# Performance work log

Measured on AMD Instinct MI355X. Metric: run time of the kernel, lower is better.

The kernel has to match this reference:

```python
import jax, jax.numpy as jnp
import numpy as np

N_NODES = 50000
N_EDGES = 800000
MUL = 32            # multiplicity of 0e and 1o feature irreps
N_SPECIES = 4       # node_attr = 4x0e one-hot
N_BASIS = 8         # radial basis scalars
N_HID = 8           # invariant_neurons
AVG_NEIGH = 16.0
INV_SQRT3 = 1.0 / np.sqrt(3.0).astype(np.float32)


def setup_inputs() -> dict:
    key = jax.random.key(0)
    ks = jax.random.split(key, 16)
    x = jax.random.normal(ks[0], (N_NODES, MUL * 4), jnp.float32)  # 32x0e + 32x1o
    species = jax.random.randint(ks[1], (N_NODES,), 0, N_SPECIES)
    node_attr = jax.nn.one_hot(species, N_SPECIES, dtype=jnp.float32)
    edge_embedding = jax.random.normal(ks[2], (N_EDGES, N_BASIS), jnp.float32)
    edge_attr = jax.random.normal(ks[3], (N_EDGES, 4), jnp.float32)  # 1x0e + 1x1o
    edge_index = jax.random.randint(ks[4], (2, N_EDGES), 0, N_NODES)
    # learned params
    W_lin1_s = jax.random.normal(ks[5], (MUL, MUL), jnp.float32)
    W_lin1_v = jax.random.normal(ks[6], (MUL, MUL), jnp.float32)
    fc_w1 = jax.random.normal(ks[7], (N_BASIS, N_HID), jnp.float32)
    fc_w2 = jax.random.normal(ks[8], (N_HID, 4 * MUL), jnp.float32)  # tp.weight_numel = 4*MUL
    W_lin2_s = jax.random.normal(ks[9], (2 * MUL, MUL), jnp.float32)  # mid simplify: 64x0e
    W_lin2_v = jax.random.normal(ks[10], (2 * MUL, MUL), jnp.float32)  # 64x1o
    W_sc_s = jax.random.normal(ks[11], (MUL, N_SPECIES, MUL), jnp.float32)
    W_sc_v = jax.random.normal(ks[12], (MUL, N_SPECIES, MUL), jnp.float32)
    return dict(node_features=x, node_attr=node_attr, edge_embedding=edge_embedding,
                edge_attr=edge_attr, edge_index=edge_index,
                W_lin1_s=W_lin1_s, W_lin1_v=W_lin1_v, fc_w1=fc_w1, fc_w2=fc_w2,
                W_lin2_s=W_lin2_s, W_lin2_v=W_lin2_v, W_sc_s=W_sc_s, W_sc_v=W_sc_v)


def _forward(node_features, node_attr, edge_embedding, edge_attr, edge_index,
             W_lin1_s, W_lin1_v, fc_w1, fc_w2, W_lin2_s, W_lin2_v, W_sc_s, W_sc_v):
    n = node_features.shape[0]
    xs = node_features[:, :MUL]                       # [N, 32] scalars (0e)
    xv = node_features[:, MUL:].reshape(n, MUL, 3)    # [N, 32, 3] vectors (1o)

    # self-connection: FullyConnectedTensorProduct(feat, 4x0e -> feat), uvw weights
    sc_norm = 1.0 / np.sqrt(MUL * N_SPECIES).astype(np.float32)
    sc_s = jnp.einsum('nu,nv,uvw->nw', xs, node_attr, W_sc_s) * sc_norm
    sc_v = jnp.einsum('nui,nv,uvw->nwi', xv, node_attr, W_sc_v) * sc_norm

    # linear_1: per-irrep channel mixing, 1/sqrt(fan_in)
    l1n = 1.0 / np.sqrt(MUL).astype(np.float32)
    ys = (xs @ W_lin1_s) * l1n
    yv = jnp.einsum('nui,uw->nwi', xv, W_lin1_v) * l1n

    # radial MLP -> per-edge tensor-product weights (4 paths x MUL)
    h = jax.nn.silu((edge_embedding @ fc_w1) / np.sqrt(N_BASIS).astype(np.float32))
    w = (h @ fc_w2) / np.sqrt(N_HID).astype(np.float32)  # [E, 128]
    w00, w01, w10, w11 = jnp.split(w, 4, axis=1)          # instruction order (0,0),(0,1),(1,0),(1,1)

    src = edge_index[0]
    dst = edge_index[1]
    es = ys[src]                                          # [E, 32]
    ev = yv[src]                                          # [E, 32, 3]
    a0 = edge_attr[:, 0]                                  # [E]    0e
    a1 = edge_attr[:, 1:4]                                # [E, 3] 1o

    # per-edge weighted uvu tensor product paths
    o_s_a = w00 * es * a0[:, None]                                       # 0e x 0e -> 0e
    o_s_b = w11 * jnp.einsum('eui,ei->eu', ev, a1) * INV_SQRT3           # 1o x 1o -> 0e
    o_v_a = (w01 * es)[:, :, None] * a1[:, None, :]                      # 0e x 1o -> 1o
    o_v_b = w10[:, :, None] * ev * a0[:, None, None]                     # 1o x 0e -> 1o

    # scatter-sum to destination nodes
    mid_s = jax.ops.segment_sum(jnp.concatenate([o_s_a, o_s_b], axis=1), dst, num_segments=n)
    mid_v = jax.ops.segment_sum(jnp.concatenate([o_v_a, o_v_b], axis=1), dst, num_segments=n)
    inv = 1.0 / np.sqrt(AVG_NEIGH).astype(np.float32)
    mid_s = mid_s * inv   # [N, 64]
    mid_v = mid_v * inv   # [N, 64, 3]

    # linear_2: 64x0e+64x1o -> 32x0e+32x1o
    l2n = 1.0 / np.sqrt(2 * MUL).astype(np.float32)
    out_s = (mid_s @ W_lin2_s) * l2n + sc_s
    out_v = jnp.einsum('nui,uw->nwi', mid_v, W_lin2_v) * l2n + sc_v
    return jnp.concatenate([out_s, out_v.reshape(n, MUL * 3)], axis=1)


def reference(node_features, node_attr, edge_embedding, edge_attr, edge_index,
              W_lin1_s, W_lin1_v, fc_w1, fc_w2, W_lin2_s, W_lin2_v, W_sc_s, W_sc_v):
    return _forward(node_features, node_attr, edge_embedding, edge_attr, edge_index,
                    W_lin1_s, W_lin1_v, fc_w1, fc_w2, W_lin2_s, W_lin2_v, W_sc_s, W_sc_v)
```

## Files before the change

### kernel.cpp

```cpp
#include <hip/hip_runtime.h>
#include <hip/hip_bf16.h>

#define N_NODES 50000
#define N_EDGES 800000
#define CAP 48
#define NODE_BLOCKS 1250
#define BUCKET_BLOCKS (N_EDGES/256)

__device__ __forceinline__ unsigned short f2bf(float f) {
    union { float f; unsigned u; } t; t.f = f;
    unsigned r = t.u + 0x7FFF + ((t.u >> 16) & 1);
    return (unsigned short)(r >> 16);
}

template<bool HP>
__global__ __launch_bounds__(256) void prep_kernel(
    const float* __restrict__ x, const float* __restrict__ attr,
    const float* __restrict__ W1s, const float* __restrict__ W1v,
    const float* __restrict__ Wscs, const float* __restrict__ Wscv,
    const float* __restrict__ ee, const float* __restrict__ eattr,
    const float* __restrict__ fcw1,
    const int* __restrict__ eidx,
    int* __restrict__ counts, int* __restrict__ bucket,
    float* __restrict__ hpay,
    unsigned short* __restrict__ ysvh, float* __restrict__ out)
{
    __shared__ float shm[9216];
    const int tid = threadIdx.x;

    if (blockIdx.x < NODE_BLOCKS) {
        const int nl = tid >> 5;
        const int w  = tid & 31;

        float w1s[32], w1v[32];
        #pragma unroll
        for (int u = 0; u < 32; ++u) {
            w1s[u] = W1s[u*32 + w];
            w1v[u] = W1v[u*32 + w];
        }
        #pragma unroll
        for (int i = 0; i < 4; ++i) {
            ((float4*)(shm + 1024))[tid + i*256] = ((const float4*)Wscs)[tid + i*256];
            ((float4*)(shm + 5120))[tid + i*256] = ((const float4*)Wscv)[tid + i*256];
        }

        const float l1n = 0.17677669529663687f;
        const float scn = 0.08838834764831843f;

        for (int batch = 0; batch < 5; ++batch) {
            const int node0 = blockIdx.x * 40 + batch * 8;
            __syncthreads();
            ((float4*)shm)[tid] = ((const float4*)(x + (long)node0 * 128))[tid];
            __syncthreads();

            const int node = node0 + nl;
            const float* at = attr + (long)node * 4;
            int sp = 0;
            if (at[1] > 0.5f) sp = 1;
            if (at[2] > 0.5f) sp = 2;
            if (at[3] > 0.5f) sp = 3;

            const float* lx   = shm + nl * 128;
            const float* lscs = shm + 1024 + sp * 32;
            const float* lscv = shm + 5120 + sp * 32;

            float ys = 0.f, yv0 = 0.f, yv1 = 0.f, yv2 = 0.f;
            float ss = 0.f, sv0 = 0.f, sv1 = 0.f, sv2 = 0.f;
            #pragma unroll
            for (int u4 = 0; u4 < 8; ++u4) {
                const float4 xs4 = ((const float4*)lx)[u4];
                const float4 q0  = ((const float4*)(lx + 32))[u4*3 + 0];
                const float4 q1  = ((const float4*)(lx + 32))[u4*3 + 1];
                const float4 q2  = ((const float4*)(lx + 32))[u4*3 + 2];
                const float xsv[4]  = {xs4.x, xs4.y, xs4.z, xs4.w};
                const float xvv[12] = {q0.x,q0.y,q0.z,q0.w,
                                       q1.x,q1.y,q1.z,q1.w,
                                       q2.x,q2.y,q2.z,q2.w};
                #pragma unroll
                for (int j = 0; j < 4; ++j) {
                    const int u = u4*4 + j;
                    const float wss = lscs[u*128 + w];
                    const float wsv = lscv[u*128 + w];
                    ys  += xsv[j] * w1s[u];
                    yv0 += xvv[3*j+0] * w1v[u];
                    yv1 += xvv[3*j+1] * w1v[u];
                    yv2 += xvv[3*j+2] * w1v[u];
                    ss  += xsv[j] * wss;
                    sv0 += xvv[3*j+0] * wsv;
                    sv1 += xvv[3*j+1] * wsv;
                    sv2 += xvv[3*j+2] * wsv;
                }
            }

            uint2 pk;
            pk.x = (unsigned)f2bf(ys  * l1n) | ((unsigned)f2bf(yv0 * l1n) << 16);
            pk.y = (unsigned)f2bf(yv1 * l1n) | ((unsigned)f2bf(yv2 * l1n) << 16);
            *(uint2*)(ysvh + (long)node * 128 + w * 4) = pk;

            float* op = out + (long)node * 128;
            op[w] = ss * scn;
            op[32 + 3*w + 0] = sv0 * scn;
            op[32 + 3*w + 1] = sv1 * scn;
            op[32 + 3*w + 2] = sv2 * scn;
        }
    } else {
        const int e = (blockIdx.x - NODE_BLOCKS) * 256 + tid;
        const int dst = eidx[N_EDGES + e];
        if (HP) {
            const int slot = atomicAdd(&counts[dst], 1);
            const float inv_sqrt8 = 0.35355339059327373f;
            const int src = eidx[e];
            const float4 ea = ((const float4*)(ee + (long)e * 8))[0];
            const float4 eb = ((const float4*)(ee + (long)e * 8))[1];
            const float4 at = ((const float4*)eattr)[e];
            const float eev[8] = {ea.x, ea.y, ea.z, ea.w, eb.x, eb.y, eb.z, eb.w};
            float h[8];
            #pragma unroll
            for (int j = 0; j < 8; ++j) {
                float pre = 0.f;
                #pragma unroll
                for (int b = 0; b < 8; ++b) pre += eev[b] * fcw1[b*8 + j];
                pre *= inv_sqrt8;
                h[j] = pre / (1.f + __expf(-pre)) * inv_sqrt8;
            }
            if (slot < CAP) {
                float4* hp = (float4*)(hpay + ((long)dst * CAP + slot) * 16);
                hp[0] = make_float4(h[0], h[1], h[2], h[3]);
                hp[1] = make_float4(h[4], h[5], h[6], h[7]);
                hp[2] = at;
                hp[3] = make_float4(__int_as_float(src), 0.f, 0.f, 0.f);
            }
        } else {
            const int slot = atomicAdd(&counts[dst], 1);
            if (slot < CAP) bucket[(long)dst * CAP + slot] = e;
        }
    }
}

template<bool HP>
__global__ __launch_bounds__(256) void agg_kernel(
    const float* __restrict__ ee, const float* __restrict__ eattr,
    const int* __restrict__ eidx,
    const float* __restrict__ fcw1, const float* __restrict__ fcw2,
    const float* __restrict__ W2s, const float* __restrict__ W2v,
    const unsigned short* __restrict__ ysvh,
    const int* __restrict__ counts, const int* __restrict__ bucket,
    const float* __restrict__ hpay,
    float* __restrict__ out)
{
    __shared__ float hrec[8][32 * 12];
    __shared__ float mid[8][256];

    const int tid = threadIdx.x;
    const int nl = tid >> 5;
    const int u  = tid & 31;
    const int node = blockIdx.x * 8 + nl;
    const float inv_sqrt8 = 0.35355339059327373f;

    float f2r[8][4];
    #pragma unroll
    for (int j = 0; j < 8; ++j) {
        f2r[j][0] = fcw2[j*128 + u];
        f2r[j][1] = fcw2[j*128 + 32 + u];
        f2r[j][2] = fcw2[j*128 + 64 + u];
        f2r[j][3] = fcw2[j*128 + 96 + u];
    }

    const int cnt = min(counts[node], CAP);
    const bool dummy = (u >= cnt);
    int s0 = 0;

    if (HP) {
        float4 p0 = make_float4(0.f,0.f,0.f,0.f);
        float4 p1 = p0, p2 = p0;
        if (!dummy) {
            const float4* hp = (const float4*)(hpay + ((long)node * CAP + u) * 16);
            p0 = hp[0]; p1 = hp[1]; p2 = hp[2];
            s0 = __float_as_int(hp[3].x);
        }
        float* hr = hrec[nl] + u * 12;
        ((float4*)hr)[0] = p0;
        ((float4*)hr)[1] = p1;
        ((float4*)hr)[2] = p2;
    } else {
        int e0 = bucket[(long)node * CAP + min(u, CAP-1)];
        if (dummy) e0 = 0;
        s0 = dummy ? 0 : eidx[e0];
        const float4 ea = ((const float4*)(ee + (long)e0 * 8))[0];
        const float4 eb = ((const float4*)(ee + (long)e0 * 8))[1];
        const float4 at = ((const float4*)eattr)[e0];
        const float eev[8] = {ea.x, ea.y, ea.z, ea.w, eb.x, eb.y, eb.z, eb.w};
        float* hr = hrec[nl] + u * 12;
        float h[8];
        #pragma unroll
        for (int j = 0; j < 8; ++j) {
            float pre = 0.f;
            #pragma unroll
            for (int b = 0; b < 8; ++b) pre += eev[b] * fcw1[b*8 + j];
            pre *= inv_sqrt8;
            const float s = pre / (1.f + __expf(-pre)) * inv_sqrt8;
            h[j] = dummy ? 0.f : s;
        }
        ((float4*)hr)[0] = make_float4(h[0], h[1], h[2], h[3]);
        ((float4*)hr)[1] = make_float4(h[4], h[5], h[6], h[7]);
        ((float4*)hr)[2] = at;
    }

    float msa = 0.f, msb = 0.f;
    float va0 = 0.f, va1 = 0.f, va2 = 0.f;
    float vb0 = 0.f, vb1 = 0.f, vb2 = 0.f;

    #define ACCUM(HA, HB, AT, Y)                                             \
    {                                                                        \
        const float es = __uint_as_float((Y).x << 16);                       \
        const float ex = __uint_as_float((Y).x & 0xffff0000u);               \
        const float ey = __uint_as_float((Y).y << 16);                       \
        const float ez = __uint_as_float((Y).y & 0xffff0000u);               \
        const float hh[8] = {HA.x,HA.y,HA.z,HA.w,HB.x,HB.y,HB.z,HB.w};       \
        float w00=0.f, w01=0.f, w10=0.f, w11=0.f;                            \
        _Pragma("unroll")                                                    \
        for (int j = 0; j < 8; ++j) {                                        \
            w00 += hh[j]*f2r[j][0]; w01 += hh[j]*f2r[j][1];                  \
            w10 += hh[j]*f2r[j][2]; w11 += hh[j]*f2r[j][3];                  \
        }                                                                    \
        const float a0 = AT.x, a1x = AT.y, a1y = AT.z, a1z = AT.w;           \
        msa += w00 * es * a0;                                                \
        msb += w11 * (ex*a1x + ey*a1y + ez*a1z);                             \
        const float t = w01 * es;                                            \
        va0 += t*a1x; va1 += t*a1y; va2 += t*a1z;                            \
        const float s = w10 * a0;                                            \
        vb0 += s*ex; vb1 += s*ey; vb2 += s*ez;                               \
    }

    #define GATHER(SLOT) \
        (*(const uint2*)(ysvh + (long)__shfl(s0, (SLOT), 32) * 128 + u * 4))

    const int c0 = min(cnt, 32);
    {
        uint2 y0 = GATHER(0), y1 = GATHER(1), y2 = GATHER(2), y3 = GATHER(3);
        for (int k = 0; k < c0; k += 4) {
            const int kn = (k + 4) & 31;
            const uint2 n0 = GATHER(kn);
            const uint2 n1 = GATHER(kn + 1);
            const uint2 n2 = GATHER(kn + 2);
            const uint2 n3 = GATHER(kn + 3);
            const float4* h0p = (const float4*)(hrec[nl] + (k + 0) * 12);
            const float4* h1p = (const float4*)(hrec[nl] + (k + 1) * 12);
            const float4* h2p = (const float4*)(hrec[nl] + (k + 2) * 12);
            const float4* h3p = (const float4*)(hrec[nl] + (k + 3) * 12);
            const float4 A0 = h0p[0], B0 = h0p[1], T0 = h0p[2];
            const float4 A1 = h1p[0], B1 = h1p[1], T1 = h1p[2];
            const float4 A2 = h2p[0], B2 = h2p[1], T2 = h2p[2];
            const float4 A3 = h3p[0], B3 = h3p[1], T3 = h3p[2];
            ACCUM(A0, B0, T0, y0)
            ACCUM(A1, B1, T1, y1)
            ACCUM(A2, B2, T2, y2)
            ACCUM(A3, B3, T3, y3)
            y0 = n0; y1 = n1; y2 = n2; y3 = n3;
        }
    }

    if (cnt > 32) {
        for (int k = 32; k < cnt; ++k) {
            float4 HA, HB, at2; int s;
            if (HP) {
                const float4* hp = (const float4*)(hpay + ((long)node * CAP + k) * 16);
                HA = hp[0]; HB = hp[1]; at2 = hp[2];
                s = __float_as_int(hp[3].x);
            } else {
                const int e = bucket[(long)node * CAP + k];
                s = eidx[e];
                const float4 ea = ((const float4*)(ee + (long)e * 8))[0];
                const float4 eb = ((const float4*)(ee + (long)e * 8))[1];
                at2 = ((const float4*)eattr)[e];
                const float eev[8] = {ea.x, ea.y, ea.z, ea.w, eb.x, eb.y, eb.z, eb.w};
                float h[8];
                #pragma unroll
                for (int j = 0; j < 8; ++j) {
                    float pre = 0.f;
                    #pragma unroll
                    for (int b = 0; b < 8; ++b) pre += eev[b] * fcw1[b*8 + j];
                    pre *= inv_sqrt8;
                    h[j] = pre / (1.f + __expf(-pre)) * inv_sqrt8;
                }
                HA = make_float4(h[0], h[1], h[2], h[3]);
                HB = make_float4(h[4], h[5], h[6], h[7]);
            }
            const uint2 y = *(const uint2*)(ysvh + (long)s * 128 + u * 4);
            ACCUM(HA, HB, at2, y)
        }
    }
    #undef GATHER
    #undef ACCUM

    msb *= 0.5773502691896258f;

    float* m = mid[nl];
    m[u]       = msa;
    m[32 + u]  = msb;
    m[64  + u*3 + 0] = va0;  m[64  + u*3 + 1] = va1;  m[64  + u*3 + 2] = va2;
    m[160 + u*3 + 0] = vb0;  m[160 + u*3 + 1] = vb1;  m[160 + u*3 + 2] = vb2;

    float os = 0.f, ov0 = 0.f, ov1 = 0.f, ov2 = 0.f;
    #pragma unroll 8
    for (int q = 0; q < 32; ++q) {
        const float wsa = W2s[q*32 + u];
        const float wsb = W2s[(32 + q)*32 + u];
        os += m[q] * wsa + m[32 + q] * wsb;
        const float wva = W2v[q*32 + u];
        const float wvb = W2v[(32 + q)*32 + u];
        ov0 += m[64 + q*3 + 0] * wva + m[160 + q*3 + 0] * wvb;
        ov1 += m[64 + q*3 + 1] * wva + m[160 + q*3 + 1] * wvb;
        ov2 += m[64 + q*3 + 2] * wva + m[160 + q*3 + 2] * wvb;
    }

    const float sc = 0.03125f;
    float* op = out + (long)node * 128;
    op[u]            += os  * sc;
    op[32 + 3*u + 0] += ov0 * sc;
    op[32 + 3*u + 1] += ov1 * sc;
    op[32 + 3*u + 2] += ov2 * sc;
}

extern "C" void kernel_launch(void* const* d_in, const int* in_sizes, int n_in,
                              void* d_out, int out_size, void* d_ws, size_t ws_size,
                              hipStream_t stream) {
    const float* x     = (const float*)d_in[0];
    const float* attr  = (const float*)d_in[1];
    const float* ee    = (const float*)d_in[2];
    const float* eattr = (const float*)d_in[3];
    const int*   eidx  = (const int*)  d_in[4];
    const float* W1s   = (const float*)d_in[5];
    const float* W1v   = (const float*)d_in[6];
    const float* fcw1  = (const float*)d_in[7];
    const float* fcw2  = (const float*)d_in[8];
    const float* W2s   = (const float*)d_in[9];
    const float* W2v   = (const float*)d_in[10];
    const float* Wscs  = (const float*)d_in[11];
    const float* Wscv  = (const float*)d_in[12];

    float* out = (float*)d_out;

    unsigned short* ysvh = (unsigned short*)d_ws;
    int*   counts = (int*)(ysvh + (long)N_NODES * 128);
    int*   bucket = counts + N_NODES;
    float* hpay   = (float*)(counts + N_NODES);

    const size_t need_hp = (size_t)N_NODES*256 + (size_t)N_NODES*4
                         + (size_t)N_NODES*CAP*64;

    hipMemsetAsync(counts, 0, N_NODES * sizeof(int), stream);
    if (ws_size >= need_hp) {
        prep_kernel<true><<<NODE_BLOCKS + BUCKET_BLOCKS, 256, 0, stream>>>(
            x, attr, W1s, W1v, Wscs, Wscv, ee, eattr, fcw1, eidx,
            counts, bucket, hpay, ysvh, out);
        agg_kernel<true><<<N_NODES/8, 256, 0, stream>>>(ee, eattr, eidx, fcw1, fcw2,
            W2s, W2v, ysvh, counts, bucket, hpay, out);
    } else {
        prep_kernel<false><<<NODE_BLOCKS + BUCKET_BLOCKS, 256, 0, stream>>>(
            x, attr, W1s, W1v, Wscs, Wscv, ee, eattr, fcw1, eidx,
            counts, bucket, hpay, ysvh, out);
        agg_kernel<false><<<N_NODES/8, 256, 0, stream>>>(ee, eattr, eidx, fcw1, fcw2,
            W2s, W2v, ysvh, counts, bucket, hpay, out);
    }
}
```

Measured before the change: 274.2 us.

## Interleave node and edge blocks in prep kernel, drop shared-memory weight staging

The prep kernel now launches one block per 8 nodes and interleaves them with edge-bucketing blocks (two node blocks for every edge block), so node and edge work share the GPU throughout instead of running as separate phases. The shared-memory staging of x and the self-connection weights is removed: each thread reads weights and node features straight from global memory (mostly cache hits), and launch bounds request 8 blocks per CU. The aim is more occupancy and less load imbalance and barrier cost, at the price of more redundant global/L2 weight reads per block.

```diff
diff --git a/kernel.cpp b/kernel.cpp
--- a/kernel.cpp
+++ b/kernel.cpp
@@ -4,8 +4,7 @@
 #define N_NODES 50000
 #define N_EDGES 800000
 #define CAP 48
-#define NODE_BLOCKS 1250
-#define BUCKET_BLOCKS (N_EDGES/256)
+#define PREP_BLOCKS 9375
 
 __device__ __forceinline__ unsigned short f2bf(float f) {
     union { float f; unsigned u; } t; t.f = f;
@@ -14,7 +13,7 @@
 }
 
 template<bool HP>
-__global__ __launch_bounds__(256) void prep_kernel(
+__global__ __launch_bounds__(256, 8) void prep_kernel(
     const float* __restrict__ x, const float* __restrict__ attr,
     const float* __restrict__ W1s, const float* __restrict__ W1v,
     const float* __restrict__ Wscs, const float* __restrict__ Wscv,
@@ -25,86 +24,72 @@
     float* __restrict__ hpay,
     unsigned short* __restrict__ ysvh, float* __restrict__ out)
 {
-    __shared__ float shm[9216];
     const int tid = threadIdx.x;
-
-    if (blockIdx.x < NODE_BLOCKS) {
+    const int b   = blockIdx.x;
+
+    if (b % 3 != 1) {
+        const int node_ord = b - (b + 2) / 3;
         const int nl = tid >> 5;
         const int w  = tid & 31;
-
-        float w1s[32], w1v[32];
-        #pragma unroll
-        for (int u = 0; u < 32; ++u) {
-            w1s[u] = W1s[u*32 + w];
-            w1v[u] = W1v[u*32 + w];
-        }
-        #pragma unroll
-        for (int i = 0; i < 4; ++i) {
-            ((float4*)(shm + 1024))[tid + i*256] = ((const float4*)Wscs)[tid + i*256];
-            ((float4*)(shm + 5120))[tid + i*256] = ((const float4*)Wscv)[tid + i*256];
-        }
+        const int node = node_ord * 8 + nl;
+
+        const float* at = attr + (long)node * 4;
+        int sp = 0;
+        if (at[1] > 0.5f) sp = 1;
+        if (at[2] > 0.5f) sp = 2;
+        if (at[3] > 0.5f) sp = 3;
+
+        const float4* xr   = (const float4*)(x + (long)node * 128);
+        const float*  gw1s = W1s + w;
+        const float*  gw1v = W1v + w;
+        const float*  gscs = Wscs + sp * 32 + w;
+        const float*  gscv = Wscv + sp * 32 + w;
 
         const float l1n = 0.17677669529663687f;
         const float scn = 0.08838834764831843f;
 
-        for (int batch = 0; batch < 5; ++batch) {
-            const int node0 = blockIdx.x * 40 + batch * 8;
-            __syncthreads();
-            ((float4*)shm)[tid] = ((const float4*)(x + (long)node0 * 128))[tid];
-            __syncthreads();
-
-            const int node = node0 + nl;
-            const float* at = attr + (long)node * 4;
-            int sp = 0;
-            if (at[1] > 0.5f) sp = 1;
-            if (at[2] > 0.5f) sp = 2;
-            if (at[3] > 0.5f) sp = 3;
-
-            const float* lx   = shm + nl * 128;
-            const float* lscs = shm + 1024 + sp * 32;
-            const float* lscv = shm + 5120 + sp * 32;
-
-            float ys = 0.f, yv0 = 0.f, yv1 = 0.f, yv2 = 0.f;
-            float ss = 0.f, sv0 = 0.f, sv1 = 0.f, sv2 = 0.f;
+        float ys = 0.f, yv0 = 0.f, yv1 = 0.f, yv2 = 0.f;
+        float ss = 0.f, sv0 = 0.f, sv1 = 0.f, sv2 = 0.f;
+        #pragma unroll
+        for (int u4 = 0; u4 < 8; ++u4) {
+            const float4 xs4 = xr[u4];
+            const float4 q0  = xr[8 + u4*3 + 0];
+            const float4 q1  = xr[8 + u4*3 + 1];
+            const float4 q2  = xr[8 + u4*3 + 2];
+            const float xsv[4]  = {xs4.x, xs4.y, xs4.z, xs4.w};
+            const float xvv[12] = {q0.x,q0.y,q0.z,q0.w,
+                                   q1.x,q1.y,q1.z,q1.w,
+                                   q2.x,q2.y,q2.z,q2.w};
             #pragma unroll
-            for (int u4 = 0; u4 < 8; ++u4) {
-                const float4 xs4 = ((const float4*)lx)[u4];
-                const float4 q0  = ((const float4*)(lx + 32))[u4*3 + 0];
-                const float4 q1  = ((const float4*)(lx + 32))[u4*3 + 1];
-                const float4 q2  = ((const float4*)(lx + 32))[u4*3 + 2];
-                const float xsv[4]  = {xs4.x, xs4.y, xs4.z, xs4.w};
-                const float xvv[12] = {q0.x,q0.y,q0.z,q0.w,
-                                       q1.x,q1.y,q1.z,q1.w,
-                                       q2.x,q2.y,q2.z,q2.w};
-                #pragma unroll
-                for (int j = 0; j < 4; ++j) {
-                    const int u = u4*4 + j;
-                    const float wss = lscs[u*128 + w];
-                    const float wsv = lscv[u*128 + w];
-                    ys  += xsv[j] * w1s[u];
-                    yv0 += xvv[3*j+0] * w1v[u];
-                    yv1 += xvv[3*j+1] * w1v[u];
-                    yv2 += xvv[3*j+2] * w1v[u];
-                    ss  += xsv[j] * wss;
-                    sv0 += xvv[3*j+0] * wsv;
-                    sv1 += xvv[3*j+1] * wsv;
-                    sv2 += xvv[3*j+2] * wsv;
-                }
+            for (int j = 0; j < 4; ++j) {
+                const int u = u4*4 + j;
+                const float w1su = gw1s[u*32];
+                const float w1vu = gw1v[u*32];
+                const float wss  = gscs[u*128];
+                const float wsv  = gscv[u*128];
+                ys  += xsv[j] * w1su;
+                yv0 += xvv[3*j+0] * w1vu;
+                yv1 += xvv[3*j+1] * w1vu;
+                yv2 += xvv[3*j+2] * w1vu;
+                ss  += xsv[j] * wss;
+                sv0 += xvv[3*j+0] * wsv;
+                sv1 += xvv[3*j+1] * wsv;
+                sv2 += xvv[3*j+2] * wsv;
             }
-
-            uint2 pk;
-            pk.x = (unsigned)f2bf(ys  * l1n) | ((unsigned)f2bf(yv0 * l1n) << 16);
-            pk.y = (unsigned)f2bf(yv1 * l1n) | ((unsigned)f2bf(yv2 * l1n) << 16);
-            *(uint2*)(ysvh + (long)node * 128 + w * 4) = pk;
-
-            float* op = out + (long)node * 128;
-            op[w] = ss * scn;
-            op[32 + 3*w + 0] = sv0 * scn;
-            op[32 + 3*w + 1] = sv1 * scn;
-            op[32 + 3*w + 2] = sv2 * scn;
-        }
+        }
+
+        uint2 pk;
+        pk.x = (unsigned)f2bf(ys  * l1n) | ((unsigned)f2bf(yv0 * l1n) << 16);
+        pk.y = (unsigned)f2bf(yv1 * l1n) | ((unsigned)f2bf(yv2 * l1n) << 16);
+        *(uint2*)(ysvh + (long)node * 128 + w * 4) = pk;
+
+        float* op = out + (long)node * 128;
+        op[w] = ss * scn;
+        op[32 + 3*w + 0] = sv0 * scn;
+        op[32 + 3*w + 1] = sv1 * scn;
+        op[32 + 3*w + 2] = sv2 * scn;
     } else {
-        const int e = (blockIdx.x - NODE_BLOCKS) * 256 + tid;
+        const int e = (b / 3) * 256 + tid;
         const int dst = eidx[N_EDGES + e];
         if (HP) {
             const int slot = atomicAdd(&counts[dst], 1);
@@ -119,7 +104,7 @@
             for (int j = 0; j < 8; ++j) {
                 float pre = 0.f;
                 #pragma unroll
-                for (int b = 0; b < 8; ++b) pre += eev[b] * fcw1[b*8 + j];
+                for (int bb = 0; bb < 8; ++bb) pre += eev[bb] * fcw1[bb*8 + j];
                 pre *= inv_sqrt8;
                 h[j] = pre / (1.f + __expf(-pre)) * inv_sqrt8;
             }
@@ -196,7 +181,7 @@
         for (int j = 0; j < 8; ++j) {
             float pre = 0.f;
             #pragma unroll
-            for (int b = 0; b < 8; ++b) pre += eev[b] * fcw1[b*8 + j];
+            for (int bb = 0; bb < 8; ++bb) pre += eev[bb] * fcw1[bb*8 + j];
             pre *= inv_sqrt8;
             const float s = pre / (1.f + __expf(-pre)) * inv_sqrt8;
             h[j] = dummy ? 0.f : s;
@@ -279,7 +264,7 @@
                 for (int j = 0; j < 8; ++j) {
                     float pre = 0.f;
                     #pragma unroll
-                    for (int b = 0; b < 8; ++b) pre += eev[b] * fcw1[b*8 + j];
+                    for (int bb = 0; bb < 8; ++bb) pre += eev[bb] * fcw1[bb*8 + j];
                     pre *= inv_sqrt8;
                     h[j] = pre / (1.f + __expf(-pre)) * inv_sqrt8;
                 }
@@ -351,13 +336,13 @@
 
     hipMemsetAsync(counts, 0, N_NODES * sizeof(int), stream);
     if (ws_size >= need_hp) {
-        prep_kernel<true><<<NODE_BLOCKS + BUCKET_BLOCKS, 256, 0, stream>>>(
+        prep_kernel<true><<<PREP_BLOCKS, 256, 0, stream>>>(
             x, attr, W1s, W1v, Wscs, Wscv, ee, eattr, fcw1, eidx,
             counts, bucket, hpay, ysvh, out);
         agg_kernel<true><<<N_NODES/8, 256, 0, stream>>>(ee, eattr, eidx, fcw1, fcw2,
             W2s, W2v, ysvh, counts, bucket, hpay, out);
     } else {
-        prep_kernel<false><<<NODE_BLOCKS + BUCKET_BLOCKS, 256, 0, stream>>>(
+        prep_kernel<false><<<PREP_BLOCKS, 256, 0, stream>>>(
             x, attr, W1s, W1v, Wscs, Wscv, ee, eattr, fcw1, eidx,
             counts, bucket, hpay, ysvh, out);
         agg_kernel<false><<<N_NODES/8, 256, 0, stream>>>(ee, eattr, eidx, fcw1, fcw2,
```

Result: slower. 383.2 us (+39.7%).
